# Kernel optimization log

Measured on AMD Instinct MI355X. Metric: run time of the kernel, lower is better.

## Reference

```python
import jax, jax.numpy as jnp
import numpy as np

B, LD = 256, 64
NO, LO = 10240, 32
NM, LM = 81920, 16
EO, EM = 81920, 327680
E, HID, H, Dh, V = 128, 256, 8, 16, 10000


def masked_mean(tokens, table):
    # tokens: [N, L] int; pad id = 0
    emb = table[tokens]                            # [N, L, E]
    mask = (tokens != 0)
    s = jnp.sum(emb * mask[..., None].astype(emb.dtype), axis=1)
    lens = jnp.maximum(jnp.sum(mask, axis=1), 1).astype(emb.dtype)
    return s / lens[:, None]


def segment_softmax(scores, seg, num_segments):
    # scores: [E, ...]; softmax over entries sharing seg id (PyG softmax)
    m = jax.ops.segment_max(scores, seg, num_segments=num_segments)
    e = jnp.exp(scores - m[seg])
    s = jax.ops.segment_sum(e, seg, num_segments=num_segments)
    return e / (s[seg] + 1e-16)


def gcn_conv(x, W, b, src, dst, n):
    # PyG GCNConv: normalize=True, add_self_loops=True
    xw = x @ W
    loops = jnp.arange(n, dtype=src.dtype)
    s2 = jnp.concatenate([src, loops])
    d2 = jnp.concatenate([dst, loops])
    deg = jax.ops.segment_sum(jnp.ones_like(d2, dtype=x.dtype), d2, num_segments=n)
    dinv = deg ** -0.5  # deg >= 1 due to self loops
    norm = dinv[s2] * dinv[d2]
    out = jax.ops.segment_sum(xw[s2] * norm[:, None], d2, num_segments=n)
    return out + b


def transformer_conv(x, Wq, bq, Wk, bk, Wv, bv, Wskip, bskip, src, dst, n):
    q = (x @ Wq + bq).reshape(n, H, Dh)
    k = (x @ Wk + bk).reshape(n, H, Dh)
    v = (x @ Wv + bv).reshape(n, H, Dh)
    score = jnp.sum(q[dst] * k[src], axis=-1) / jnp.sqrt(jnp.asarray(Dh, x.dtype))  # [E, H]
    alpha = segment_softmax(score, dst, n)
    agg = jax.ops.segment_sum(alpha[:, :, None] * v[src], dst, num_segments=n)  # [n, H, Dh]
    return agg.reshape(n, H * Dh) + x @ Wskip + bskip


def global_attention(x, Wg, bg, seg, num_segments):
    gate = x @ Wg + bg                              # [N, 1]
    a = segment_softmax(gate, seg, num_segments)
    return jax.ops.segment_sum(a * x, seg, num_segments=num_segments)


def setup_inputs():
    key = jax.random.key(0)
    ks = jax.random.split(key, 20)
    sc = lambda k, shape: jax.random.normal(k, shape, dtype=jnp.float32) * 0.05
    inp = {
        "desc_tokens": jax.random.randint(ks[0], (B, LD), 0, V, dtype=jnp.int32),
        "x_tokens": jax.random.randint(ks[1], (NO, LO), 0, V, dtype=jnp.int32),
        "mini_tokens": jax.random.randint(ks[2], (NM, LM), 0, V, dtype=jnp.int32),
        "src": jax.random.randint(ks[3], (EO,), 0, NO, dtype=jnp.int32),
        "dst": jax.random.randint(ks[4], (EO,), 0, NO, dtype=jnp.int32),
        "mini_src": jax.random.randint(ks[5], (EM,), 0, NM, dtype=jnp.int32),
        "mini_dst": jax.random.randint(ks[6], (EM,), 0, NM, dtype=jnp.int32),
        "mini_batch": (jnp.arange(NM, dtype=jnp.int32) // (NM // NO)),
        "node_batch": (jnp.arange(NO, dtype=jnp.int32) // (NO // B)),
        "desc_table": sc(ks[7], (V, E)),
        "code_table": sc(ks[8], (V, E)),
        "code_table2": sc(ks[9], (V, E)),
        "Wq": sc(ks[10], (E, H * Dh)), "bq": jnp.zeros((H * Dh,), jnp.float32),
        "Wk": sc(ks[11], (E, H * Dh)), "bk": jnp.zeros((H * Dh,), jnp.float32),
        "Wv": sc(ks[12], (E, H * Dh)), "bv": jnp.zeros((H * Dh,), jnp.float32),
        "Wskip": sc(ks[13], (E, H * Dh)), "bskip": jnp.zeros((H * Dh,), jnp.float32),
        "W2": sc(ks[14], (E, HID)), "b2": jnp.zeros((HID,), jnp.float32),
        "W3": sc(ks[15], (HID, E)), "b3": jnp.zeros((E,), jnp.float32),
        "Wg": sc(ks[16], (E, 1)), "bg": jnp.zeros((1,), jnp.float32),
    }
    return inp


def reference(desc_tokens, x_tokens, mini_tokens, src, dst, mini_src, mini_dst,
              mini_batch, node_batch, desc_table, code_table, code_table2,
              Wq, bq, Wk, bk, Wv, bv, Wskip, bskip, W2, b2, W3, b3, Wg, bg):
    # encode_desc: embedding + masked mean pool -> [B, E]
    h_n = masked_mean(desc_tokens, desc_table)
    # encode_code_graph
    stmt_emb = masked_mean(x_tokens, code_table2)          # [NO, E]
    mini_emb = masked_mean(mini_tokens, code_table)        # [NM, E]
    mini_hidden = transformer_conv(mini_emb, Wq, bq, Wk, bk, Wv, bv,
                                   Wskip, bskip, mini_src, mini_dst, NM)
    mini_fn = global_attention(mini_hidden, Wg, bg, mini_batch, NO)  # [NO, E]
    mini_fn = (mini_fn + stmt_emb) * 0.5
    h = jax.nn.relu(gcn_conv(mini_fn, W2, b2, src, dst, NO))
    final_stmt = gcn_conv(h, W3, b3, src, dst, NO)
    fn_repr = global_attention(final_stmt, Wg, bg, node_batch, B)    # [B, E]
    # cosine similarity (torch eps=1e-8 clamps each norm)
    na = jnp.maximum(jnp.linalg.norm(fn_repr, axis=-1), 1e-8)
    nb = jnp.maximum(jnp.linalg.norm(h_n, axis=-1), 1e-8)
    return jnp.sum(fn_repr * h_n, axis=-1) / (na * nb)
```

## Files before the change

kernel.cpp:

```cpp
#include <hip/hip_runtime.h>
#include <hip/hip_bf16.h>
#include <math.h>

#define BB   256
#define LDE  64
#define NO   10240
#define LO   32
#define NM   81920
#define LM   16
#define EO   81920
#define EM   327680
#define ED   128
#define HIDD 256
#define NH   8
#define DH   16
#define VV   10000

static inline int nblk(long long n, int b) { return (int)((n + b - 1) / b); }

typedef __attribute__((ext_vector_type(8))) short short8;
typedef __attribute__((ext_vector_type(4))) float f32x4;

static __device__ __forceinline__ unsigned short bf16_rne(float f) {
  unsigned u = __float_as_uint(f);
  return (unsigned short)((u + 0x7fffu + ((u >> 16) & 1u)) >> 16);
}
static __device__ __forceinline__ float bf16_to_f(unsigned short h) {
  return __uint_as_float(((unsigned)h) << 16);
}
static __device__ __forceinline__ float4 b4f(ushort4 h) {
  return make_float4(bf16_to_f(h.x), bf16_to_f(h.y), bf16_to_f(h.z), bf16_to_f(h.w));
}

struct WC { const float* W; int K, M; short8* hi; short8* lo; int base; };
struct WC6 { WC w[6]; };
__global__ void __launch_bounds__(256)
conv_all_k(WC6 wc, const float* __restrict__ t1, unsigned short* __restrict__ o1,
           const float* __restrict__ t2, unsigned short* __restrict__ o2) {
  if (blockIdx.x < 64) {
    int g = blockIdx.x * 256 + threadIdx.x;
    int wi = 0;
    #pragma unroll
    for (int i = 1; i < 6; ++i) if (g >= wc.w[i].base) wi = i;
    const WC c = wc.w[wi];
    int idx = g - c.base;
    int lane = idx & 63;
    int nt = (idx >> 6) % (c.M / 16);
    int kb = (idx >> 6) / (c.M / 16);
    int n = nt * 16 + (lane & 15);
    int k0 = kb * 32 + ((lane >> 4) << 3);
    short8 h, l;
    #pragma unroll
    for (int j = 0; j < 8; ++j) {
      float v = c.W[(size_t)(k0 + j) * c.M + n];
      unsigned short hb = bf16_rne(v);
      h[j] = (short)hb;
      l[j] = (short)bf16_rne(v - bf16_to_f(hb));
    }
    c.hi[idx] = h; c.lo[idx] = l;
  } else {
    int q = (blockIdx.x - 64) * 256 + threadIdx.x;
    const int NT = VV * ED / 4;
    if (q < NT) {
      float4 v = *(const float4*)(t1 + (size_t)q * 4);
      *(ushort4*)(o1 + (size_t)q * 4) =
          make_ushort4(bf16_rne(v.x), bf16_rne(v.y), bf16_rne(v.z), bf16_rne(v.w));
    } else if (q < 2 * NT) {
      int q2 = q - NT;
      float4 v = *(const float4*)(t2 + (size_t)q2 * 4);
      *(ushort4*)(o2 + (size_t)q2 * 4) =
          make_ushort4(bf16_rne(v.x), bf16_rne(v.y), bf16_rne(v.z), bf16_rne(v.w));
    }
  }
}

template<int L, bool TBF, bool OUTBF>
static __device__ __forceinline__ void embed_body(const int* __restrict__ tokens,
                                                  const void* __restrict__ table,
                                                  void* __restrict__ out, int blk) {
  const int r = threadIdx.x >> 5, lane = threadIdx.x & 31;
  const int n0 = blk * 8;
  __shared__ int toks[8][L];
  for (int i = threadIdx.x; i < 8 * L; i += 256)
    toks[i / L][i % L] = tokens[(size_t)n0 * L + i];
  __syncthreads();
  float4 acc = make_float4(0.f, 0.f, 0.f, 0.f);
  int cnt = 0;
  #pragma unroll
  for (int l = 0; l < L; ++l) {
    int t = toks[r][l];
    float4 v;
    if (TBF) v = b4f(*((const ushort4*)((const unsigned short*)table + (size_t)t * ED + lane * 4)));
    else     v = *(const float4*)((const float*)table + (size_t)t * ED + lane * 4);
    float msk = (t != 0) ? 1.f : 0.f;
    cnt += (t != 0);
    acc.x = fmaf(msk, v.x, acc.x); acc.y = fmaf(msk, v.y, acc.y);
    acc.z = fmaf(msk, v.z, acc.z); acc.w = fmaf(msk, v.w, acc.w);
  }
  float inv = 1.f / (float)(cnt > 0 ? cnt : 1);
  acc.x *= inv; acc.y *= inv; acc.z *= inv; acc.w *= inv;
  if (OUTBF)
    *(ushort4*)((unsigned short*)out + (size_t)(n0 + r) * ED + lane * 4) =
        make_ushort4(bf16_rne(acc.x), bf16_rne(acc.y), bf16_rne(acc.z), bf16_rne(acc.w));
  else
    *(float4*)((float*)out + (size_t)(n0 + r) * ED + lane * 4) = acc;
}

__global__ void __launch_bounds__(256)
embed_all_k(const int* __restrict__ desc_tokens, const float* __restrict__ desc_table,
            float* __restrict__ h_n,
            const int* __restrict__ x_tokens, const unsigned short* __restrict__ ctab2,
            float* __restrict__ stmt,
            const int* __restrict__ mini_tokens, const unsigned short* __restrict__ ctab,
            unsigned short* __restrict__ miniE) {
  int b = blockIdx.x;
  if (b < BB / 8) embed_body<LDE, false, false>(desc_tokens, desc_table, h_n, b);
  else if (b < BB / 8 + NO / 8) embed_body<LO, true, false>(x_tokens, ctab2, stmt, b - BB / 8);
  else embed_body<LM, true, true>(mini_tokens, ctab, miniE, b - BB / 8 - NO / 8);
}

struct QDesc { const short8* bh; const float* bias; unsigned short* C; };
struct QDesc4 { QDesc d[4]; };

__global__ void __launch_bounds__(512)
mgemm_qkvs6_k(const unsigned short* __restrict__ Ab, QDesc4 g4) {
  const QDesc d = g4.d[blockIdx.x];
  const int n0 = blockIdx.y * 128;
  const int tid = threadIdx.x;
  const int w = tid >> 6, lane = tid & 63;
  const int wm = (w & 3) * 2;
  const int wn = (w >> 2) * 4;
  const int r = lane & 15, qd = lane >> 4;
  f32x4 acc[2][4];
  #pragma unroll
  for (int i = 0; i < 2; ++i)
    #pragma unroll
    for (int j = 0; j < 4; ++j) acc[i][j] = (f32x4){0.f, 0.f, 0.f, 0.f};
  #pragma unroll
  for (int kb = 0; kb < 4; ++kb) {
    short8 bh[4];
    #pragma unroll
    for (int j = 0; j < 4; ++j)
      bh[j] = d.bh[((size_t)kb * 8 + wn + j) * 64 + lane];
    short8 a[2];
    #pragma unroll
    for (int i = 0; i < 2; ++i)
      a[i] = *(const short8*)(Ab + (size_t)(n0 + (wm + i) * 16 + r) * ED + kb * 32 + qd * 8);
    #pragma unroll
    for (int i = 0; i < 2; ++i)
      #pragma unroll
      for (int j = 0; j < 4; ++j)
        acc[i][j] = __builtin_amdgcn_mfma_f32_16x16x32_bf16(a[i], bh[j], acc[i][j], 0, 0, 0);
  }
  #pragma unroll
  for (int i = 0; i < 2; ++i)
    #pragma unroll
    for (int j = 0; j < 4; ++j) {
      int col = (wn + j) * 16 + r;
      float bv = d.bias[col];
      #pragma unroll
      for (int rr = 0; rr < 4; ++rr) {
        int row = (wm + i) * 16 + qd * 4 + rr;
        d.C[(size_t)(n0 + row) * ED + col] = bf16_rne(acc[i][j][rr] + bv);
      }
    }
}

template<bool RELU>
__global__ void __launch_bounds__(256)
mgemm_k(const float* __restrict__ A, const short8* __restrict__ Bh,
        const short8* __restrict__ Bl, const float* __restrict__ bias,
        float* C, int K, int M) {
  __shared__ short8 Ah[8][64];
  __shared__ short8 Al[8][64];
  const int bm0 = blockIdx.y * 128, bn0 = blockIdx.x * 128;
  const int tid = threadIdx.x;
  const int w = tid >> 6, lane = tid & 63;
  const int wm = (w & 1) * 4, wn = (w >> 1) * 4;
  const int NTm = M / 16;
  f32x4 acc[4][4];
  #pragma unroll
  for (int i = 0; i < 4; ++i)
    #pragma unroll
    for (int j = 0; j < 4; ++j) acc[i][j] = (f32x4){0.f, 0.f, 0.f, 0.f};
  const int kbn = K / 32;
  for (int kb = 0; kb < kbn; ++kb) {
    __syncthreads();
    #pragma unroll
    for (int it = 0; it < 2; ++it) {
      int u = tid + it * 256;
      int mt = u >> 6, l = u & 63;
      int m = bm0 + mt * 16 + (l & 15);
      int k = kb * 32 + ((l >> 4) << 3);
      const float* ap = A + (size_t)m * K + k;
      float4 v0 = *(const float4*)ap;
      float4 v1 = *(const float4*)(ap + 4);
      float f[8] = {v0.x, v0.y, v0.z, v0.w, v1.x, v1.y, v1.z, v1.w};
      short8 hh, ll;
      #pragma unroll
      for (int j = 0; j < 8; ++j) {
        unsigned short hb = bf16_rne(f[j]);
        hh[j] = (short)hb;
        ll[j] = (short)bf16_rne(f[j] - bf16_to_f(hb));
      }
      Ah[mt][l] = hh; Al[mt][l] = ll;
    }
    __syncthreads();
    short8 bh[4], bl[4];
    #pragma unroll
    for (int j = 0; j < 4; ++j) {
      size_t bi = ((size_t)kb * NTm + (bn0 >> 4) + wn + j) * 64 + lane;
      bh[j] = Bh[bi]; bl[j] = Bl[bi];
    }
    #pragma unroll
    for (int i = 0; i < 4; ++i) {
      short8 ah = Ah[wm + i][lane];
      short8 al = Al[wm + i][lane];
      #pragma unroll
      for (int j = 0; j < 4; ++j) {
        acc[i][j] = __builtin_amdgcn_mfma_f32_16x16x32_bf16(ah, bh[j], acc[i][j], 0, 0, 0);
        acc[i][j] = __builtin_amdgcn_mfma_f32_16x16x32_bf16(ah, bl[j], acc[i][j], 0, 0, 0);
        acc[i][j] = __builtin_amdgcn_mfma_f32_16x16x32_bf16(al, bh[j], acc[i][j], 0, 0, 0);
      }
    }
  }
  const int q = lane >> 4, c = lane & 15;
  #pragma unroll
  for (int i = 0; i < 4; ++i)
    #pragma unroll
    for (int j = 0; j < 4; ++j) {
      int col = bn0 + (wn + j) * 16 + c;
      float bv = bias ? bias[col] : 0.f;
      #pragma unroll
      for (int rr = 0; rr < 4; ++rr) {
        int row = bm0 + (wm + i) * 16 + q * 4 + rr;
        float v = acc[i][j][rr] + bv;
        if (RELU) v = fmaxf(v, 0.f);
        C[(size_t)row * M + col] = v;
      }
    }
}

__global__ void hist2_k(const int* __restrict__ dm, int* __restrict__ hm,
                        const int* __restrict__ dd, int* __restrict__ ho) {
  int e = blockIdx.x * 256 + threadIdx.x;
  if (e < EM) atomicAdd(&hm[dm[e]], 1);
  else { int e2 = e - EM; if (e2 < EO) atomicAdd(&ho[dd[e2]], 1); }
}
__global__ void chunk_sum_k(const int* __restrict__ hist, int* __restrict__ partials, int N) {
  __shared__ int sd[256];
  int i = blockIdx.x * 256 + threadIdx.x;
  sd[threadIdx.x] = (i < N) ? hist[i] : 0;
  __syncthreads();
  for (int s = 128; s > 0; s >>= 1) {
    if (threadIdx.x < s) sd[threadIdx.x] += sd[threadIdx.x + s];
    __syncthreads();
  }
  if (threadIdx.x == 0) partials[blockIdx.x] = sd[0];
}
__global__ void scan_partials2_k(int* __restrict__ p) {
  __shared__ int sd[512];
  int base = (blockIdx.x == 0) ? 0 : NM / 256;
  int B    = (blockIdx.x == 0) ? NM / 256 : NO / 256;
  int t = threadIdx.x;
  int v = (t < B) ? p[base + t] : 0;
  sd[t] = v; __syncthreads();
  for (int off = 1; off < 512; off <<= 1) {
    int a = (t >= off) ? sd[t - off] : 0;
    __syncthreads();
    sd[t] += a;
    __syncthreads();
  }
  if (t < B) p[base + t] = sd[t] - v;
}
__global__ void scan_final2_k(const int* __restrict__ hist, const int* __restrict__ partials,
                              int* __restrict__ offsm, int* __restrict__ curm,
                              int* __restrict__ offso, int* __restrict__ curo,
                              float* __restrict__ dinv) {
  __shared__ int sd[256];
  int i = blockIdx.x * 256 + threadIdx.x;
  int v = hist[i];
  sd[threadIdx.x] = v; __syncthreads();
  for (int off = 1; off < 256; off <<= 1) {
    int a = (threadIdx.x >= off) ? sd[threadIdx.x - off] : 0;
    __syncthreads();
    sd[threadIdx.x] += a;
    __syncthreads();
  }
  int excl = sd[threadIdx.x] - v + partials[blockIdx.x];
  if (i < NM) {
    offsm[i] = excl; curm[i] = excl;
    if (i == NM - 1) offsm[NM] = excl + v;
  } else {
    int i2 = i - NM;
    offso[i2] = excl; curo[i2] = excl;
    if (i2 == NO - 1) offso[NO] = excl + v;
    dinv[i2] = 1.f / sqrtf(1.f + (float)v);
  }
}
__global__ void scatter2_k(const int* __restrict__ sm, const int* __restrict__ dm,
                           int* __restrict__ cm, int* __restrict__ km,
                           const int* __restrict__ so, const int* __restrict__ dd,
                           int* __restrict__ co, int* __restrict__ ko) {
  int e = blockIdx.x * 256 + threadIdx.x;
  if (e < EM) {
    int pos = atomicAdd(&cm[dm[e]], 1);
    km[pos] = sm[e];
  } else {
    int e2 = e - EM;
    if (e2 < EO) {
      int pos = atomicAdd(&co[dd[e2]], 1);
      ko[pos] = so[e2];
    }
  }
}

__global__ void __launch_bounds__(128)
attn_fused_k(unsigned short* qh, const unsigned short* __restrict__ kk,
             const unsigned short* __restrict__ vv, const unsigned short* __restrict__ skip,
             const int* __restrict__ offs, const int* __restrict__ csr,
             const float* __restrict__ Wg, const float* __restrict__ bg,
             float* __restrict__ gateOut) {
  const int g = threadIdx.x >> 5, lane = threadIdx.x & 31;
  const int n = blockIdx.x * 4 + g;
  float4 q = b4f(*(const ushort4*)(qh + (size_t)n * ED + lane * 4));
  int lo = offs[n], hi = offs[n + 1];
  float4 O = make_float4(0.f, 0.f, 0.f, 0.f);
  float m = -INFINITY, l = 0.f;
  for (int base = lo; base < hi; base += 4) {
    int rem = hi - base;
    int sidx[4];
    #pragma unroll
    for (int i = 0; i < 4; ++i) sidx[i] = (i < rem) ? csr[base + i] : 0;
    ushort4 kr[4], vr[4];
    #pragma unroll
    for (int i = 0; i < 4; ++i) {
      kr[i] = *(const ushort4*)(kk + (size_t)sidx[i] * ED + lane * 4);
      vr[i] = *(const ushort4*)(vv + (size_t)sidx[i] * ED + lane * 4);
    }
    #pragma unroll
    for (int i = 0; i < 4; ++i) {
      float4 kt = b4f(kr[i]);
      float4 vt = b4f(vr[i]);
      float p = q.x * kt.x + q.y * kt.y + q.z * kt.z + q.w * kt.w;
      p += __shfl_xor(p, 1, 64);
      p += __shfl_xor(p, 2, 64);
      float sc = (i < rem) ? p * 0.25f : -INFINITY;
      float mn = fmaxf(m, sc);
      float scale = __expf(m - mn);
      float pe = __expf(sc - mn);
      l = l * scale + pe;
      O.x = O.x * scale + pe * vt.x; O.y = O.y * scale + pe * vt.y;
      O.z = O.z * scale + pe * vt.z; O.w = O.w * scale + pe * vt.w;
      m = mn;
    }
  }
  float inv = 1.f / (l + 1e-16f);
  float4 sk = b4f(*(const ushort4*)(skip + (size_t)n * ED + lane * 4));
  float4 out = make_float4(O.x * inv + sk.x, O.y * inv + sk.y,
                           O.z * inv + sk.z, O.w * inv + sk.w);
  *(ushort4*)(qh + (size_t)n * ED + lane * 4) =
      make_ushort4(bf16_rne(out.x), bf16_rne(out.y), bf16_rne(out.z), bf16_rne(out.w));
  float4 wg = *(const float4*)(Wg + lane * 4);
  float ps = out.x * wg.x + out.y * wg.y + out.z * wg.z + out.w * wg.w;
  #pragma unroll
  for (int o = 1; o <= 16; o <<= 1) ps += __shfl_xor(ps, o, 64);
  if (lane == 0) gateOut[n] = ps + bg[0];
}

__global__ void __launch_bounds__(128)
gcn_gather_k(const float* __restrict__ x, const float* __restrict__ dinv,
             const int* __restrict__ offs, const int* __restrict__ csr,
             const float* __restrict__ bias, float* __restrict__ out,
             const float* __restrict__ Wg, const float* __restrict__ bg,
             float* __restrict__ gateOut) {
  const int g = threadIdx.x >> 5, lane = threadIdx.x & 31;
  const int n = blockIdx.x * 4 + g;
  float di = dinv[n];
  float4 xs = *(const float4*)(x + (size_t)n * ED + lane * 4);
  float w0 = di * di;
  float4 acc = make_float4(w0 * xs.x, w0 * xs.y, w0 * xs.z, w0 * xs.w);
  int lo = offs[n], hi = offs[n + 1];
  for (int base = lo; base < hi; base += 4) {
    int rem = hi - base;
    int sidx[4];
    #pragma unroll
    for (int i = 0; i < 4; ++i) sidx[i] = (i < rem) ? csr[base + i] : 0;
    float dw[4];
    #pragma unroll
    for (int i = 0; i < 4; ++i) dw[i] = (i < rem) ? di * dinv[sidx[i]] : 0.f;
    float4 vr[4];
    #pragma unroll
    for (int i = 0; i < 4; ++i)
      vr[i] = *(const float4*)(x + (size_t)sidx[i] * ED + lane * 4);
    #pragma unroll
    for (int i = 0; i < 4; ++i) {
      acc.x = fmaf(dw[i], vr[i].x, acc.x); acc.y = fmaf(dw[i], vr[i].y, acc.y);
      acc.z = fmaf(dw[i], vr[i].z, acc.z); acc.w = fmaf(dw[i], vr[i].w, acc.w);
    }
  }
  if (bias) {
    float4 b4 = *(const float4*)(bias + lane * 4);
    acc.x += b4.x; acc.y += b4.y; acc.z += b4.z; acc.w += b4.w;
  }
  *(float4*)(out + (size_t)n * ED + lane * 4) = acc;
  if (gateOut) {
    float4 wg = *(const float4*)(Wg + lane * 4);
    float ps = acc.x * wg.x + acc.y * wg.y + acc.z * wg.z + acc.w * wg.w;
    #pragma unroll
    for (int o = 1; o <= 16; o <<= 1) ps += __shfl_xor(ps, o, 64);
    if (lane == 0) gateOut[n] = ps + bg[0];
  }
}

static __device__ __forceinline__ int lower_bound_d(const int* a, int n, int key) {
  int lo = 0, hi = n;
  while (lo < hi) { int mid = (lo + hi) >> 1; if (a[mid] < key) lo = mid + 1; else hi = mid; }
  return lo;
}
template<bool COMBINE, bool XBF>
__global__ void __launch_bounds__(128)
gattn_k(const void* __restrict__ xv, const float* __restrict__ gate,
        const int* __restrict__ seg, int Ntot,
        const float* __restrict__ other, float* __restrict__ out) {
  const int g = threadIdx.x >> 5, lane = threadIdx.x & 31;
  const int n = blockIdx.x * 4 + g;
  __shared__ int sh[4][2];
  if (lane == 0) {
    sh[g][0] = lower_bound_d(seg, Ntot, n);
    sh[g][1] = lower_bound_d(seg, Ntot, n + 1);
  }
  __syncthreads();
  int lo = sh[g][0], hi = sh[g][1];
  float m = -INFINITY;
  for (int j = lo; j < hi; ++j) m = fmaxf(m, gate[j]);
  float ssum = 0.f;
  for (int j = lo; j < hi; ++j) ssum += __expf(gate[j] - m);
  float inv = 1.f / (ssum + 1e-16f);
  float4 acc = make_float4(0.f, 0.f, 0.f, 0.f);
  for (int j = lo; j < hi; ++j) {
    float a = __expf(gate[j] - m) * inv;
    float4 v;
    if (XBF) v = b4f(*((const ushort4*)((const unsigned short*)xv + (size_t)j * ED + lane * 4)));
    else     v = *((const float4*)((const float*)xv + (size_t)j * ED) + lane);
    acc.x = fmaf(a, v.x, acc.x); acc.y = fmaf(a, v.y, acc.y);
    acc.z = fmaf(a, v.z, acc.z); acc.w = fmaf(a, v.w, acc.w);
  }
  if (COMBINE) {
    float4 o4 = *(const float4*)(other + (size_t)n * ED + lane * 4);
    acc.x = (acc.x + o4.x) * 0.5f; acc.y = (acc.y + o4.y) * 0.5f;
    acc.z = (acc.z + o4.z) * 0.5f; acc.w = (acc.w + o4.w) * 0.5f;
  }
  *(float4*)(out + (size_t)n * ED + lane * 4) = acc;
}

__global__ void __launch_bounds__(128)
gattn_cos_k(const float* __restrict__ x, const float* __restrict__ gate,
            const int* __restrict__ seg, int Ntot,
            const float* __restrict__ hn, float* __restrict__ outp) {
  const int g = threadIdx.x >> 5, lane = threadIdx.x & 31;
  const int n = blockIdx.x * 4 + g;
  __shared__ int sh[4][2];
  if (lane == 0) {
    sh[g][0] = lower_bound_d(seg, Ntot, n);
    sh[g][1] = lower_bound_d(seg, Ntot, n + 1);
  }
  __syncthreads();
  int lo = sh[g][0], hi = sh[g][1];
  float m = -INFINITY;
  for (int j = lo; j < hi; ++j) m = fmaxf(m, gate[j]);
  float ssum = 0.f;
  for (int j = lo; j < hi; ++j) ssum += __expf(gate[j] - m);
  float inv = 1.f / (ssum + 1e-16f);
  float4 acc = make_float4(0.f, 0.f, 0.f, 0.f);
  for (int j = lo; j < hi; ++j) {
    float a = __expf(gate[j] - m) * inv;
    float4 v = *((const float4*)(x + (size_t)j * ED) + lane);
    acc.x = fmaf(a, v.x, acc.x); acc.y = fmaf(a, v.y, acc.y);
    acc.z = fmaf(a, v.z, acc.z); acc.w = fmaf(a, v.w, acc.w);
  }
  float4 hv = *(const float4*)(hn + (size_t)n * ED + lane * 4);
  float dot = acc.x * hv.x + acc.y * hv.y + acc.z * hv.z + acc.w * hv.w;
  float na  = acc.x * acc.x + acc.y * acc.y + acc.z * acc.z + acc.w * acc.w;
  float nb  = hv.x * hv.x + hv.y * hv.y + hv.z * hv.z + hv.w * hv.w;
  #pragma unroll
  for (int o = 1; o <= 16; o <<= 1) {
    dot += __shfl_xor(dot, o, 64);
    na  += __shfl_xor(na,  o, 64);
    nb  += __shfl_xor(nb,  o, 64);
  }
  if (lane == 0)
    outp[n] = dot / (fmaxf(sqrtf(na), 1e-8f) * fmaxf(sqrtf(nb), 1e-8f));
}

constexpr size_t OFF_HN    = 0;
constexpr size_t OFF_STMT  = OFF_HN    + (size_t)BB * ED;
constexpr size_t OFF_A     = OFF_STMT  + (size_t)NO * ED;
constexpr size_t OFF_QHID  = OFF_A     + (size_t)NM * ED;
constexpr size_t OFF_CT    = OFF_QHID  + (size_t)NM * ED / 2;
constexpr size_t OFF_K     = OFF_QHID  + (size_t)NM * ED;
constexpr size_t OFF_V     = OFF_K     + (size_t)NM * ED;
constexpr size_t T0        = OFF_V     + (size_t)NM * ED;
constexpr size_t OFF_GATE  = T0;
constexpr size_t OFF_GATE2 = OFF_GATE  + (size_t)NM;
constexpr size_t OFF_DINV  = OFF_GATE2 + (size_t)NO;
constexpr size_t OFF_HISTM = OFF_DINV  + (size_t)NO;
constexpr size_t OFF_HISTO = OFF_HISTM + (size_t)NM;
constexpr size_t OFF_OFFSM = OFF_HISTO + (size_t)NO;
constexpr size_t OFF_CURM  = OFF_OFFSM + (size_t)NM + 1;
constexpr size_t OFF_CSRM  = OFF_CURM  + (size_t)NM;
constexpr size_t OFF_OFFSO = OFF_CSRM  + (size_t)EM;
constexpr size_t OFF_CURO  = OFF_OFFSO + (size_t)NO + 1;
constexpr size_t OFF_CSRO  = OFF_CURO  + (size_t)NO;
constexpr size_t OFF_PART  = OFF_CSRO  + (size_t)EO;
constexpr size_t OFF_WFHI  = OFF_PART  + 512;
constexpr size_t OFF_WFLO  = OFF_WFHI  + 65536;
constexpr size_t WO_Q  = 0, WO_K = 2048, WO_V = 4096, WO_S = 6144, WO_W2 = 8192, WO_W3 = 12288;
constexpr size_t OFF_MFN   = OFF_A;
constexpr size_t OFF_AGG   = OFF_MFN   + (size_t)NO * ED;
constexpr size_t OFF_H     = OFF_AGG   + (size_t)NO * ED;
constexpr size_t OFF_T     = OFF_H     + (size_t)NO * HIDD;
constexpr size_t OFF_FIN   = OFF_T     + (size_t)NO * ED;

extern "C" void kernel_launch(void* const* d_in, const int* in_sizes, int n_in,
                              void* d_out, int out_size, void* d_ws, size_t ws_size,
                              hipStream_t stream) {
  const int* desc_tokens = (const int*)d_in[0];
  const int* x_tokens    = (const int*)d_in[1];
  const int* mini_tokens = (const int*)d_in[2];
  const int* src         = (const int*)d_in[3];
  const int* dst         = (const int*)d_in[4];
  const int* mini_src    = (const int*)d_in[5];
  const int* mini_dst    = (const int*)d_in[6];
  const int* mini_batch  = (const int*)d_in[7];
  const int* node_batch  = (const int*)d_in[8];
  const float* desc_table  = (const float*)d_in[9];
  const float* code_table  = (const float*)d_in[10];
  const float* code_table2 = (const float*)d_in[11];
  const float* Wq = (const float*)d_in[12]; const float* bq = (const float*)d_in[13];
  const float* Wk = (const float*)d_in[14]; const float* bk = (const float*)d_in[15];
  const float* Wv = (const float*)d_in[16]; const float* bv = (const float*)d_in[17];
  const float* Wskip = (const float*)d_in[18]; const float* bskip = (const float*)d_in[19];
  const float* W2 = (const float*)d_in[20]; const float* b2 = (const float*)d_in[21];
  const float* W3 = (const float*)d_in[22]; const float* b3 = (const float*)d_in[23];
  const float* Wg = (const float*)d_in[24]; const float* bg = (const float*)d_in[25];

  float* ws = (float*)d_ws;
  float* h_n   = ws + OFF_HN;
  float* stmt  = ws + OFF_STMT;
  unsigned short* miniE_b = (unsigned short*)(ws + OFF_A);
  unsigned short* qhid_b = (unsigned short*)(ws + OFF_QHID);
  unsigned short* ctab_b  = (unsigned short*)(ws + OFF_CT);
  unsigned short* ctab2_b = (unsigned short*)(ws + OFF_CT + (size_t)VV * ED / 2);
  unsigned short* kbuf_b = (unsigned short*)(ws + OFF_K);
  unsigned short* skip_b = kbuf_b + (size_t)NM * ED;
  unsigned short* vbuf_b = (unsigned short*)(ws + OFF_V);
  float* gate  = ws + OFF_GATE;
  float* gate2 = ws + OFF_GATE2;
  float* dinv  = ws + OFF_DINV;
  int* histm = (int*)(ws + OFF_HISTM);
  int* histo = (int*)(ws + OFF_HISTO);
  int* offsm = (int*)(ws + OFF_OFFSM);
  int* curm  = (int*)(ws + OFF_CURM);
  int* csrm  = (int*)(ws + OFF_CSRM);
  int* offso = (int*)(ws + OFF_OFFSO);
  int* curo  = (int*)(ws + OFF_CURO);
  int* csro  = (int*)(ws + OFF_CSRO);
  int* part  = (int*)(ws + OFF_PART);
  short8* wfhi = (short8*)(ws + OFF_WFHI);
  short8* wflo = (short8*)(ws + OFF_WFLO);
  float* mini_fn = ws + OFF_MFN;
  float* aggb    = ws + OFF_AGG;
  float* hbuf    = ws + OFF_H;
  float* tbuf    = ws + OFF_T;
  float* finalS  = ws + OFF_FIN;
  float* outp    = (float*)d_out;

  WC6 wc;
  wc.w[0] = {Wq,    ED,   ED,   wfhi + WO_Q,  wflo + WO_Q,  (int)WO_Q};
  wc.w[1] = {Wk,    ED,   ED,   wfhi + WO_K,  wflo + WO_K,  (int)WO_K};
  wc.w[2] = {Wv,    ED,   ED,   wfhi + WO_V,  wflo + WO_V,  (int)WO_V};
  wc.w[3] = {Wskip, ED,   ED,   wfhi + WO_S,  wflo + WO_S,  (int)WO_S};
  wc.w[4] = {W2,    ED,   HIDD, wfhi + WO_W2, wflo + WO_W2, (int)WO_W2};
  wc.w[5] = {W3,    HIDD, ED,   wfhi + WO_W3, wflo + WO_W3, (int)WO_W3};
  conv_all_k<<<64 + nblk(2 * VV * ED / 4, 256), 256, 0, stream>>>(
      wc, code_table, ctab_b, code_table2, ctab2_b);

  hipMemsetAsync(histm, 0, (size_t)(NM + NO) * 4, stream);
  hist2_k<<<nblk(EM + EO, 256), 256, 0, stream>>>(mini_dst, histm, dst, histo);
  chunk_sum_k<<<(NM + NO) / 256, 256, 0, stream>>>(histm, part, NM + NO);
  scan_partials2_k<<<2, 512, 0, stream>>>(part);
  scan_final2_k<<<(NM + NO) / 256, 256, 0, stream>>>(histm, part, offsm, curm,
                                                     offso, curo, dinv);
  scatter2_k<<<nblk(EM + EO, 256), 256, 0, stream>>>(mini_src, mini_dst, curm, csrm,
                                                     src, dst, curo, csro);

  embed_all_k<<<BB / 8 + NO / 8 + NM / 8, 256, 0, stream>>>(
      desc_tokens, desc_table, h_n, x_tokens, ctab2_b, stmt,
      mini_tokens, ctab_b, miniE_b);

  QDesc4 g4;
  g4.d[0] = {wfhi + WO_Q, bq,    qhid_b};
  g4.d[1] = {wfhi + WO_K, bk,    kbuf_b};
  g4.d[2] = {wfhi + WO_V, bv,    vbuf_b};
  g4.d[3] = {wfhi + WO_S, bskip, skip_b};
  { dim3 g(4, NM / 128); mgemm_qkvs6_k<<<g, 512, 0, stream>>>(miniE_b, g4); }

  attn_fused_k<<<NM / 4, 128, 0, stream>>>(qhid_b, kbuf_b, vbuf_b, skip_b,
                                           offsm, csrm, Wg, bg, gate);

  gattn_k<true, true><<<NO / 4, 128, 0, stream>>>(qhid_b, gate, mini_batch, NM, stmt, mini_fn);

  gcn_gather_k<<<NO / 4, 128, 0, stream>>>(mini_fn, dinv, offso, csro, nullptr, aggb,
                                           nullptr, nullptr, nullptr);
  { dim3 g(HIDD / 128, NO / 128);
    mgemm_k<true><<<g, 256, 0, stream>>>(aggb, wfhi + WO_W2, wflo + WO_W2, b2, hbuf, ED, HIDD); }

  { dim3 g(1, NO / 128);
    mgemm_k<false><<<g, 256, 0, stream>>>(hbuf, wfhi + WO_W3, wflo + WO_W3, nullptr, tbuf, HIDD, ED); }
  gcn_gather_k<<<NO / 4, 128, 0, stream>>>(tbuf, dinv, offso, csro, b3, finalS, Wg, bg, gate2);

  gattn_cos_k<<<BB / 4, 128, 0, stream>>>(finalS, gate2, node_batch, NO, h_n, outp);
}
```

Measured before the change: 367.1 us.

## Store GCN-stage intermediates in bf16 and drop split-precision GEMM

```diff
diff --git a/kernel.cpp b/kernel.cpp
--- a/kernel.cpp
+++ b/kernel.cpp
@@ -31,6 +31,9 @@
 static __device__ __forceinline__ float4 b4f(ushort4 h) {
   return make_float4(bf16_to_f(h.x), bf16_to_f(h.y), bf16_to_f(h.z), bf16_to_f(h.w));
 }
+static __device__ __forceinline__ ushort4 f4b(float4 v) {
+  return make_ushort4(bf16_rne(v.x), bf16_rne(v.y), bf16_rne(v.z), bf16_rne(v.w));
+}
 
 struct WC { const float* W; int K, M; short8* hi; short8* lo; int base; };
 struct WC6 { WC w[6]; };
@@ -63,13 +66,11 @@
     const int NT = VV * ED / 4;
     if (q < NT) {
       float4 v = *(const float4*)(t1 + (size_t)q * 4);
-      *(ushort4*)(o1 + (size_t)q * 4) =
-          make_ushort4(bf16_rne(v.x), bf16_rne(v.y), bf16_rne(v.z), bf16_rne(v.w));
+      *(ushort4*)(o1 + (size_t)q * 4) = f4b(v);
     } else if (q < 2 * NT) {
       int q2 = q - NT;
       float4 v = *(const float4*)(t2 + (size_t)q2 * 4);
-      *(ushort4*)(o2 + (size_t)q2 * 4) =
-          make_ushort4(bf16_rne(v.x), bf16_rne(v.y), bf16_rne(v.z), bf16_rne(v.w));
+      *(ushort4*)(o2 + (size_t)q2 * 4) = f4b(v);
     }
   }
 }
@@ -100,8 +101,7 @@
   float inv = 1.f / (float)(cnt > 0 ? cnt : 1);
   acc.x *= inv; acc.y *= inv; acc.z *= inv; acc.w *= inv;
   if (OUTBF)
-    *(ushort4*)((unsigned short*)out + (size_t)(n0 + r) * ED + lane * 4) =
-        make_ushort4(bf16_rne(acc.x), bf16_rne(acc.y), bf16_rne(acc.z), bf16_rne(acc.w));
+    *(ushort4*)((unsigned short*)out + (size_t)(n0 + r) * ED + lane * 4) = f4b(acc);
   else
     *(float4*)((float*)out + (size_t)(n0 + r) * ED + lane * 4) = acc;
 }
@@ -110,12 +110,12 @@
 embed_all_k(const int* __restrict__ desc_tokens, const float* __restrict__ desc_table,
             float* __restrict__ h_n,
             const int* __restrict__ x_tokens, const unsigned short* __restrict__ ctab2,
-            float* __restrict__ stmt,
+            unsigned short* __restrict__ stmt,
             const int* __restrict__ mini_tokens, const unsigned short* __restrict__ ctab,
             unsigned short* __restrict__ miniE) {
   int b = blockIdx.x;
   if (b < BB / 8) embed_body<LDE, false, false>(desc_tokens, desc_table, h_n, b);
-  else if (b < BB / 8 + NO / 8) embed_body<LO, true, false>(x_tokens, ctab2, stmt, b - BB / 8);
+  else if (b < BB / 8 + NO / 8) embed_body<LO, true, true>(x_tokens, ctab2, stmt, b - BB / 8);
   else embed_body<LM, true, true>(mini_tokens, ctab, miniE, b - BB / 8 - NO / 8);
 }
 
@@ -123,9 +123,12 @@
 struct QDesc4 { QDesc d[4]; };
 
 __global__ void __launch_bounds__(512)
-mgemm_qkvs6_k(const unsigned short* __restrict__ Ab, QDesc4 g4) {
-  const QDesc d = g4.d[blockIdx.x];
-  const int n0 = blockIdx.y * 128;
+mgemm_qkvs7_k(const unsigned short* __restrict__ Ab, QDesc4 g4) {
+  const int id = blockIdx.x;
+  const int mat = (id >> 3) & 3;
+  const int rowb = (id & 7) | ((id >> 5) << 3);
+  const QDesc d = g4.d[mat];
+  const int n0 = rowb * 128;
   const int tid = threadIdx.x;
   const int w = tid >> 6, lane = tid & 63;
   const int wm = (w & 3) * 2;
@@ -167,76 +170,50 @@
 }
 
 template<bool RELU>
-__global__ void __launch_bounds__(256)
-mgemm_k(const float* __restrict__ A, const short8* __restrict__ Bh,
-        const short8* __restrict__ Bl, const float* __restrict__ bias,
-        float* C, int K, int M) {
-  __shared__ short8 Ah[8][64];
-  __shared__ short8 Al[8][64];
-  const int bm0 = blockIdx.y * 128, bn0 = blockIdx.x * 128;
+__global__ void __launch_bounds__(512)
+mgemm_b_k(const unsigned short* __restrict__ Ab, const short8* __restrict__ Bh,
+          const float* __restrict__ bias, unsigned short* __restrict__ C,
+          int K, int M) {
+  const int bn0 = blockIdx.x * 128;
+  const int n0 = blockIdx.y * 128;
   const int tid = threadIdx.x;
   const int w = tid >> 6, lane = tid & 63;
-  const int wm = (w & 1) * 4, wn = (w >> 1) * 4;
+  const int wm = (w & 3) * 2, wn = (w >> 2) * 4;
+  const int r = lane & 15, qd = lane >> 4;
   const int NTm = M / 16;
-  f32x4 acc[4][4];
-  #pragma unroll
-  for (int i = 0; i < 4; ++i)
+  f32x4 acc[2][4];
+  #pragma unroll
+  for (int i = 0; i < 2; ++i)
     #pragma unroll
     for (int j = 0; j < 4; ++j) acc[i][j] = (f32x4){0.f, 0.f, 0.f, 0.f};
   const int kbn = K / 32;
   for (int kb = 0; kb < kbn; ++kb) {
-    __syncthreads();
-    #pragma unroll
-    for (int it = 0; it < 2; ++it) {
-      int u = tid + it * 256;
-      int mt = u >> 6, l = u & 63;
-      int m = bm0 + mt * 16 + (l & 15);
-      int k = kb * 32 + ((l >> 4) << 3);
-      const float* ap = A + (size_t)m * K + k;
-      float4 v0 = *(const float4*)ap;
-      float4 v1 = *(const float4*)(ap + 4);
-      float f[8] = {v0.x, v0.y, v0.z, v0.w, v1.x, v1.y, v1.z, v1.w};
-      short8 hh, ll;
+    short8 bh[4];
+    #pragma unroll
+    for (int j = 0; j < 4; ++j)
+      bh[j] = Bh[((size_t)kb * NTm + (bn0 >> 4) + wn + j) * 64 + lane];
+    short8 a[2];
+    #pragma unroll
+    for (int i = 0; i < 2; ++i)
+      a[i] = *(const short8*)(Ab + (size_t)(n0 + (wm + i) * 16 + r) * K + kb * 32 + qd * 8);
+    #pragma unroll
+    for (int i = 0; i < 2; ++i)
       #pragma unroll
-      for (int j = 0; j < 8; ++j) {
-        unsigned short hb = bf16_rne(f[j]);
-        hh[j] = (short)hb;
-        ll[j] = (short)bf16_rne(f[j] - bf16_to_f(hb));
-      }
-      Ah[mt][l] = hh; Al[mt][l] = ll;
-    }
-    __syncthreads();
-    short8 bh[4], bl[4];
+      for (int j = 0; j < 4; ++j)
+        acc[i][j] = __builtin_amdgcn_mfma_f32_16x16x32_bf16(a[i], bh[j], acc[i][j], 0, 0, 0);
+  }
+  #pragma unroll
+  for (int i = 0; i < 2; ++i)
     #pragma unroll
     for (int j = 0; j < 4; ++j) {
-      size_t bi = ((size_t)kb * NTm + (bn0 >> 4) + wn + j) * 64 + lane;
-      bh[j] = Bh[bi]; bl[j] = Bl[bi];
-    }
-    #pragma unroll
-    for (int i = 0; i < 4; ++i) {
-      short8 ah = Ah[wm + i][lane];
-      short8 al = Al[wm + i][lane];
-      #pragma unroll
-      for (int j = 0; j < 4; ++j) {
-        acc[i][j] = __builtin_amdgcn_mfma_f32_16x16x32_bf16(ah, bh[j], acc[i][j], 0, 0, 0);
-        acc[i][j] = __builtin_amdgcn_mfma_f32_16x16x32_bf16(ah, bl[j], acc[i][j], 0, 0, 0);
-        acc[i][j] = __builtin_amdgcn_mfma_f32_16x16x32_bf16(al, bh[j], acc[i][j], 0, 0, 0);
-      }
-    }
-  }
-  const int q = lane >> 4, c = lane & 15;
-  #pragma unroll
-  for (int i = 0; i < 4; ++i)
-    #pragma unroll
-    for (int j = 0; j < 4; ++j) {
-      int col = bn0 + (wn + j) * 16 + c;
+      int col = bn0 + (wn + j) * 16 + r;
       float bv = bias ? bias[col] : 0.f;
       #pragma unroll
       for (int rr = 0; rr < 4; ++rr) {
-        int row = bm0 + (wm + i) * 16 + q * 4 + rr;
+        int row = n0 + (wm + i) * 16 + qd * 4 + rr;
         float v = acc[i][j][rr] + bv;
         if (RELU) v = fmaxf(v, 0.f);
-        C[(size_t)row * M + col] = v;
+        C[(size_t)row * M + col] = bf16_rne(v);
       }
     }
 }
@@ -359,8 +336,7 @@
   float4 sk = b4f(*(const ushort4*)(skip + (size_t)n * ED + lane * 4));
   float4 out = make_float4(O.x * inv + sk.x, O.y * inv + sk.y,
                            O.z * inv + sk.z, O.w * inv + sk.w);
-  *(ushort4*)(qh + (size_t)n * ED + lane * 4) =
-      make_ushort4(bf16_rne(out.x), bf16_rne(out.y), bf16_rne(out.z), bf16_rne(out.w));
+  *(ushort4*)(qh + (size_t)n * ED + lane * 4) = f4b(out);
   float4 wg = *(const float4*)(Wg + lane * 4);
   float ps = out.x * wg.x + out.y * wg.y + out.z * wg.z + out.w * wg.w;
   #pragma unroll
@@ -369,15 +345,15 @@
 }
 
 __global__ void __launch_bounds__(128)
-gcn_gather_k(const float* __restrict__ x, const float* __restrict__ dinv,
-             const int* __restrict__ offs, const int* __restrict__ csr,
-             const float* __restrict__ bias, float* __restrict__ out,
-             const float* __restrict__ Wg, const float* __restrict__ bg,
-             float* __restrict__ gateOut) {
+gcn_gather_b_k(const unsigned short* __restrict__ x, const float* __restrict__ dinv,
+               const int* __restrict__ offs, const int* __restrict__ csr,
+               const float* __restrict__ bias, unsigned short* __restrict__ out,
+               const float* __restrict__ Wg, const float* __restrict__ bg,
+               float* __restrict__ gateOut) {
   const int g = threadIdx.x >> 5, lane = threadIdx.x & 31;
   const int n = blockIdx.x * 4 + g;
   float di = dinv[n];
-  float4 xs = *(const float4*)(x + (size_t)n * ED + lane * 4);
+  float4 xs = b4f(*(const ushort4*)(x + (size_t)n * ED + lane * 4));
   float w0 = di * di;
   float4 acc = make_float4(w0 * xs.x, w0 * xs.y, w0 * xs.z, w0 * xs.w);
   int lo = offs[n], hi = offs[n + 1];
@@ -389,21 +365,22 @@
     float dw[4];
     #pragma unroll
     for (int i = 0; i < 4; ++i) dw[i] = (i < rem) ? di * dinv[sidx[i]] : 0.f;
-    float4 vr[4];
+    ushort4 vr[4];
     #pragma unroll
     for (int i = 0; i < 4; ++i)
-      vr[i] = *(const float4*)(x + (size_t)sidx[i] * ED + lane * 4);
+      vr[i] = *(const ushort4*)(x + (size_t)sidx[i] * ED + lane * 4);
     #pragma unroll
     for (int i = 0; i < 4; ++i) {
-      acc.x = fmaf(dw[i], vr[i].x, acc.x); acc.y = fmaf(dw[i], vr[i].y, acc.y);
-      acc.z = fmaf(dw[i], vr[i].z, acc.z); acc.w = fmaf(dw[i], vr[i].w, acc.w);
+      float4 v = b4f(vr[i]);
+      acc.x = fmaf(dw[i], v.x, acc.x); acc.y = fmaf(dw[i], v.y, acc.y);
+      acc.z = fmaf(dw[i], v.z, acc.z); acc.w = fmaf(dw[i], v.w, acc.w);
     }
   }
   if (bias) {
     float4 b4 = *(const float4*)(bias + lane * 4);
     acc.x += b4.x; acc.y += b4.y; acc.z += b4.z; acc.w += b4.w;
   }
-  *(float4*)(out + (size_t)n * ED + lane * 4) = acc;
+  *(ushort4*)(out + (size_t)n * ED + lane * 4) = f4b(acc);
   if (gateOut) {
     float4 wg = *(const float4*)(Wg + lane * 4);
     float ps = acc.x * wg.x + acc.y * wg.y + acc.z * wg.z + acc.w * wg.w;
@@ -418,11 +395,10 @@
   while (lo < hi) { int mid = (lo + hi) >> 1; if (a[mid] < key) lo = mid + 1; else hi = mid; }
   return lo;
 }
-template<bool COMBINE, bool XBF>
 __global__ void __launch_bounds__(128)
-gattn_k(const void* __restrict__ xv, const float* __restrict__ gate,
-        const int* __restrict__ seg, int Ntot,
-        const float* __restrict__ other, float* __restrict__ out) {
+gattn_comb_b_k(const unsigned short* __restrict__ xv, const float* __restrict__ gate,
+               const int* __restrict__ seg, int Ntot,
+               const unsigned short* __restrict__ other, unsigned short* __restrict__ out) {
   const int g = threadIdx.x >> 5, lane = threadIdx.x & 31;
   const int n = blockIdx.x * 4 + g;
   __shared__ int sh[4][2];
@@ -440,22 +416,18 @@
   float4 acc = make_float4(0.f, 0.f, 0.f, 0.f);
   for (int j = lo; j < hi; ++j) {
     float a = __expf(gate[j] - m) * inv;
-    float4 v;
-    if (XBF) v = b4f(*((const ushort4*)((const unsigned short*)xv + (size_t)j * ED + lane * 4)));
-    else     v = *((const float4*)((const float*)xv + (size_t)j * ED) + lane);
+    float4 v = b4f(*(const ushort4*)(xv + (size_t)j * ED + lane * 4));
     acc.x = fmaf(a, v.x, acc.x); acc.y = fmaf(a, v.y, acc.y);
     acc.z = fmaf(a, v.z, acc.z); acc.w = fmaf(a, v.w, acc.w);
   }
-  if (COMBINE) {
-    float4 o4 = *(const float4*)(other + (size_t)n * ED + lane * 4);
-    acc.x = (acc.x + o4.x) * 0.5f; acc.y = (acc.y + o4.y) * 0.5f;
-    acc.z = (acc.z + o4.z) * 0.5f; acc.w = (acc.w + o4.w) * 0.5f;
-  }
-  *(float4*)(out + (size_t)n * ED + lane * 4) = acc;
+  float4 o4 = b4f(*(const ushort4*)(other + (size_t)n * ED + lane * 4));
+  acc.x = (acc.x + o4.x) * 0.5f; acc.y = (acc.y + o4.y) * 0.5f;
+  acc.z = (acc.z + o4.z) * 0.5f; acc.w = (acc.w + o4.w) * 0.5f;
+  *(ushort4*)(out + (size_t)n * ED + lane * 4) = f4b(acc);
 }
 
 __global__ void __launch_bounds__(128)
-gattn_cos_k(const float* __restrict__ x, const float* __restrict__ gate,
+gattn_cos_k(const unsigned short* __restrict__ x, const float* __restrict__ gate,
             const int* __restrict__ seg, int Ntot,
             const float* __restrict__ hn, float* __restrict__ outp) {
   const int g = threadIdx.x >> 5, lane = threadIdx.x & 31;
@@ -475,7 +447,7 @@
   float4 acc = make_float4(0.f, 0.f, 0.f, 0.f);
   for (int j = lo; j < hi; ++j) {
     float a = __expf(gate[j] - m) * inv;
-    float4 v = *((const float4*)(x + (size_t)j * ED) + lane);
+    float4 v = b4f(*(const ushort4*)(x + (size_t)j * ED + lane * 4));
     acc.x = fmaf(a, v.x, acc.x); acc.y = fmaf(a, v.y, acc.y);
     acc.z = fmaf(a, v.z, acc.z); acc.w = fmaf(a, v.w, acc.w);
   }
@@ -547,7 +519,7 @@
 
   float* ws = (float*)d_ws;
   float* h_n   = ws + OFF_HN;
-  float* stmt  = ws + OFF_STMT;
+  unsigned short* stmt_b  = (unsigned short*)(ws + OFF_STMT);
   unsigned short* miniE_b = (unsigned short*)(ws + OFF_A);
   unsigned short* qhid_b = (unsigned short*)(ws + OFF_QHID);
   unsigned short* ctab_b  = (unsigned short*)(ws + OFF_CT);
@@ -569,11 +541,11 @@
   int* part  = (int*)(ws + OFF_PART);
   short8* wfhi = (short8*)(ws + OFF_WFHI);
   short8* wflo = (short8*)(ws + OFF_WFLO);
-  float* mini_fn = ws + OFF_MFN;
-  float* aggb    = ws + OFF_AGG;
-  float* hbuf    = ws + OFF_H;
-  float* tbuf    = ws + OFF_T;
-  float* finalS  = ws + OFF_FIN;
+  unsigned short* mini_fn_b = (unsigned short*)(ws + OFF_MFN);
+  unsigned short* aggb_b    = (unsigned short*)(ws + OFF_AGG);
+  unsigned short* hbuf_b    = (unsigned short*)(ws + OFF_H);
+  unsigned short* tbuf_b    = (unsigned short*)(ws + OFF_T);
+  unsigned short* finalS_b  = (unsigned short*)(ws + OFF_FIN);
   float* outp    = (float*)d_out;
 
   WC6 wc;
@@ -596,7 +568,7 @@
                                                      src, dst, curo, csro);
 
   embed_all_k<<<BB / 8 + NO / 8 + NM / 8, 256, 0, stream>>>(
-      desc_tokens, desc_table, h_n, x_tokens, ctab2_b, stmt,
+      desc_tokens, desc_table, h_n, x_tokens, ctab2_b, stmt_b,
       mini_tokens, ctab_b, miniE_b);
 
   QDesc4 g4;
@@ -604,21 +576,23 @@
   g4.d[1] = {wfhi + WO_K, bk,    kbuf_b};
   g4.d[2] = {wfhi + WO_V, bv,    vbuf_b};
   g4.d[3] = {wfhi + WO_S, bskip, skip_b};
-  { dim3 g(4, NM / 128); mgemm_qkvs6_k<<<g, 512, 0, stream>>>(miniE_b, g4); }
+  mgemm_qkvs7_k<<<4 * (NM / 128), 512, 0, stream>>>(miniE_b, g4);
 
   attn_fused_k<<<NM / 4, 128, 0, stream>>>(qhid_b, kbuf_b, vbuf_b, skip_b,
                                            offsm, csrm, Wg, bg, gate);
 
-  gattn_k<true, true><<<NO / 4, 128, 0, stream>>>(qhid_b, gate, mini_batch, NM, stmt, mini_fn);
-
-  gcn_gather_k<<<NO / 4, 128, 0, stream>>>(mini_fn, dinv, offso, csro, nullptr, aggb,
-                                           nullptr, nullptr, nullptr);
+  gattn_comb_b_k<<<NO / 4, 128, 0, stream>>>(qhid_b, gate, mini_batch, NM,
+                                             stmt_b, mini_fn_b);
+
+  gcn_gather_b_k<<<NO / 4, 128, 0, stream>>>(mini_fn_b, dinv, offso, csro, nullptr,
+                                             aggb_b, nullptr, nullptr, nullptr);
   { dim3 g(HIDD / 128, NO / 128);
-    mgemm_k<true><<<g, 256, 0, stream>>>(aggb, wfhi + WO_W2, wflo + WO_W2, b2, hbuf, ED, HIDD); }
+    mgemm_b_k<true><<<g, 512, 0, stream>>>(aggb_b, wfhi + WO_W2, b2, hbuf_b, ED, HIDD); }
 
   { dim3 g(1, NO / 128);
-    mgemm_k<false><<<g, 256, 0, stream>>>(hbuf, wfhi + WO_W3, wflo + WO_W3, nullptr, tbuf, HIDD, ED); }
-  gcn_gather_k<<<NO / 4, 128, 0, stream>>>(tbuf, dinv, offso, csro, b3, finalS, Wg, bg, gate2);
-
-  gattn_cos_k<<<BB / 4, 128, 0, stream>>>(finalS, gate2, node_batch, NO, h_n, outp);
-}
+    mgemm_b_k<false><<<g, 512, 0, stream>>>(hbuf_b, wfhi + WO_W3, nullptr, tbuf_b, HIDD, ED); }
+  gcn_gather_b_k<<<NO / 4, 128, 0, stream>>>(tbuf_b, dinv, offso, csro, b3, finalS_b,
+                                             Wg, bg, gate2);
+
+  gattn_cos_k<<<BB / 4, 128, 0, stream>>>(finalS_b, gate2, node_batch, NO, h_n, outp);
+}
```

After: 350.6 us. 4.5% less time.
